# Kernel optimization log

Hardware: AMD Instinct MI355X
Metric: run time of the kernel (lower is better)

## Reference

```python
import jax, jax.numpy as jnp
import numpy as np

INPUT_DIM = 2048
N_TREES = 15
TREE_DEPTH = 3
N_LEAVES = 2 ** TREE_DEPTH          # 8
N_INTERNAL = 2 ** TREE_DEPTH - 1    # 7
PARAM_PER_TREE = N_INTERNAL * (INPUT_DIM + 1) + N_LEAVES * 2  # 14375
BATCH = 32768


def setup_inputs() -> dict:
    key = jax.random.key(0)
    k1, k2, k3 = jax.random.split(key, 3)
    x = jax.random.normal(k1, (BATCH, INPUT_DIM), dtype=jnp.float32)
    tree_params = jax.random.normal(k2, (1, N_TREES * PARAM_PER_TREE), dtype=jnp.float32)
    tree_weights = jax.random.uniform(k3, (1, N_TREES), dtype=jnp.float32)
    return {"x": x, "tree_params": tree_params, "tree_weights": tree_weights}


def reference(x, tree_params, tree_weights):
    D, T, I, L = INPUT_DIM, N_TREES, N_INTERNAL, N_LEAVES
    B = x.shape[0]
    p = tree_params[0].reshape(T, PARAM_PER_TREE)
    split_w = p[:, : I * D].reshape(T, I, D)                       # [T, I, D]
    split_b = p[:, I * D : I * (D + 1)]                            # [T, I]
    leaf_logits = p[:, I * (D + 1) :].reshape(T, L, 2)             # [T, L, 2]

    # One fused GEMM over all trees/nodes: [B, T, I]
    decisions = jax.nn.sigmoid(jnp.einsum('bd,tid->bti', x, split_w) + split_b)

    # Faithful replication of the original gating loop (leaf 0 ungated,
    # internal nodes with child index >= L are no-ops).
    leaf_probs = jnp.ones((B, T, L), dtype=x.dtype)
    for i in range(I):
        left, right = 2 * i + 1, 2 * i + 2
        d = decisions[:, :, i]
        if left < L:
            leaf_probs = leaf_probs.at[:, :, left].multiply(d)
        if right < L:
            leaf_probs = leaf_probs.at[:, :, right].multiply(1.0 - d)

    leaf_probs = leaf_probs / (leaf_probs.sum(axis=-1, keepdims=True) + 1e-8)
    leaf_dist = jax.nn.softmax(leaf_logits, axis=-1)               # [T, L, 2]
    tree_out = jnp.einsum('btl,tlc->btc', leaf_probs, leaf_dist)   # [B, T, 2]
    final_probs = jnp.einsum('btc,t->bc', tree_out, tree_weights[0])
    return final_probs
```

## Files before the change

kernel.cpp:

```cpp
#include <hip/hip_runtime.h>
#include <stdint.h>

#define D_IN    2048
#define NT      15
#define PPT     14359
#define NVALID  60

typedef __bf16   bf16x8 __attribute__((ext_vector_type(8)));
typedef float    f32x4  __attribute__((ext_vector_type(4)));
typedef uint32_t u32x4  __attribute__((ext_vector_type(4)));

#define WAITV8 asm volatile("s_waitcnt vmcnt(8)" ::: "memory")
#define WAITV0 asm volatile("s_waitcnt vmcnt(0)" ::: "memory")
#define WAITL0 asm volatile("s_waitcnt lgkmcnt(0)" ::: "memory")

__global__ __launch_bounds__(256) void prep_split(const float* __restrict__ tp,
                                                  const float* __restrict__ tw,
                                                  unsigned short* __restrict__ bsp,
                                                  float* __restrict__ bias,
                                                  float* __restrict__ coef) {
  int id = blockIdx.x * 256 + threadIdx.x;
  int n = id >> 11;
  int k = id & 2047;
  float v = 0.0f;
  if (n < NVALID) {
    int t = n >> 2, i = n & 3;
    v = tp[t * PPT + i * D_IN + k];
  }
  uint32_t u  = __float_as_uint(v);
  uint32_t hm = u & 0xFFFF0000u;
  float    lo = v - __uint_as_float(hm);
  uint32_t lu = __float_as_uint(lo);
  int ks = k >> 5, f = n >> 4;
  int lane = (n & 15) | (((k >> 3) & 3) << 4);
  int j = k & 7;
  size_t base = ((size_t)(ks * 4 + f) * 2) * 512 + (size_t)lane * 8 + j;
  bsp[base]       = (unsigned short)(u  >> 16);
  bsp[base + 512] = (unsigned short)(lu >> 16);

  if (blockIdx.x == 0) {
    int tid = threadIdx.x;
    if (tid < 64) {
      float b = 0.0f;
      if (tid < NVALID) { int t = tid >> 2, i = tid & 3; b = tp[t * PPT + 14336 + i]; }
      bias[tid] = b;
    } else if (tid < 64 + NT) {
      int t = tid - 64;
      const float* ll = tp + t * PPT + 14343;
      float d0[8], d1[8];
#pragma unroll
      for (int le = 0; le < 8; ++le) {
        float aa = ll[2 * le], bb = ll[2 * le + 1];
        float m = fmaxf(aa, bb);
        float e0 = __expf(aa - m), e1 = __expf(bb - m);
        float inv = 1.0f / (e0 + e1);
        d0[le] = e0 * inv; d1[le] = e1 * inv;
      }
      float w = tw[t];
      float* c = coef + t * 10;
      c[0] = w * (d0[0] + d0[2] + d0[4] + d0[6]);
      c[1] = w * (d1[0] + d1[2] + d1[4] + d1[6]);
      c[2] = w * (d0[1] - d0[2]);
      c[3] = w * (d1[1] - d1[2]);
      c[4] = w * (d0[3] - d0[4]);
      c[5] = w * (d1[3] - d1[4]);
      c[6] = w * (d0[5] - d0[6]);
      c[7] = w * (d1[5] - d1[6]);
      c[8] = w * d0[7];
      c[9] = w * d1[7];
    }
  }
}

__device__ __forceinline__ f32x4 gload4(const float* p) {
  f32x4 r;
  asm volatile("global_load_dwordx4 %0, %1, off" : "=v"(r) : "v"(p) : "memory");
  return r;
}
__device__ __forceinline__ u32x4 dsread16(uint32_t addr) {
  u32x4 r;
  asm volatile("ds_read_b128 %0, %1" : "=v"(r) : "v"(addr) : "memory");
  return r;
}
__device__ __forceinline__ void stage16(const void* g, void* l) {
  __builtin_amdgcn_global_load_lds(
      (const __attribute__((address_space(1))) void*)g,
      (__attribute__((address_space(3))) void*)l, 16, 0, 0);
}

#define CVT_PAIR(P, Q, HW, LW) do {                                   \
    uint32_t _up = __float_as_uint(P), _uq = __float_as_uint(Q);      \
    uint32_t _mp = _up & 0xFFFF0000u, _mq = _uq & 0xFFFF0000u;        \
    (HW) = (_up >> 16) | _mq;                                         \
    float _lp = (P) - __uint_as_float(_mp);                           \
    float _lq = (Q) - __uint_as_float(_mq);                           \
    (LW) = (__float_as_uint(_lp) >> 16) |                             \
           (__float_as_uint(_lq) & 0xFFFF0000u);                      \
  } while (0)

__device__ __forceinline__ void cvt_hilo(const f32x4 A, const f32x4 B,
                                         bf16x8& hi, bf16x8& lo) {
  u32x4 hw, lw;
  CVT_PAIR(A[0], A[1], hw[0], lw[0]);
  CVT_PAIR(A[2], A[3], hw[1], lw[1]);
  CVT_PAIR(B[0], B[1], hw[2], lw[2]);
  CVT_PAIR(B[2], B[3], hw[3], lw[3]);
  hi = __builtin_bit_cast(bf16x8, hw);
  lo = __builtin_bit_cast(bf16x8, lw);
}

#define ITERATION(tt, BUF, RC, WAIT8, ISSUE)                                   \
  {                                                                            \
    if (WAIT8) { WAITV8; } else { WAITV0; }                                    \
    __builtin_amdgcn_sched_barrier(0);                                         \
    __builtin_amdgcn_s_barrier();                                              \
    const uint32_t bb = sbase + (BUF) * 16384 + l16;                           \
    u32x4 bf[16];                                                              \
    _Pragma("unroll")                                                          \
    for (int h = 0; h < 2; ++h)                                                \
      _Pragma("unroll")                                                        \
      for (int f = 0; f < 4; ++f)                                              \
        _Pragma("unroll")                                                      \
        for (int p2 = 0; p2 < 2; ++p2)                                         \
          bf[h * 8 + f * 2 + p2] = dsread16(bb + h * 8192 + f * 2048 + p2 * 1024); \
    bf16x8 ah0, al0, ah1, al1;                                                 \
    cvt_hilo(RC[0], RC[1], ah0, al0);                                          \
    cvt_hilo(RC[2], RC[3], ah1, al1);                                          \
    WAITL0;                                                                    \
    __builtin_amdgcn_sched_barrier(0);                                         \
    if (ISSUE) {                                                               \
      const int t2 = (tt) + 2;                                                 \
      const char* gsrc = bspb + (size_t)t2 * 16384 + w4096l16;                 \
      char* ldst = sBgen + (((BUF) + 2) % 3) * 16384 + w4096;                  \
      _Pragma("unroll")                                                        \
      for (int q = 0; q < 4; ++q) stage16(gsrc + q * 1024, ldst + q * 1024);   \
      const float* ap = xbase + t2 * 64;                                       \
      RC[0] = gload4(ap);      RC[1] = gload4(ap + 4);                         \
      RC[2] = gload4(ap + 32); RC[3] = gload4(ap + 36);                        \
    }                                                                          \
    _Pragma("unroll")                                                          \
    for (int f = 0; f < 4; ++f) {                                              \
      bf16x8 bh = __builtin_bit_cast(bf16x8, bf[f * 2]);                       \
      bf16x8 bl = __builtin_bit_cast(bf16x8, bf[f * 2 + 1]);                   \
      acc[f] = __builtin_amdgcn_mfma_f32_16x16x32_bf16(ah0, bh, acc[f], 0,0,0);\
      acc[f] = __builtin_amdgcn_mfma_f32_16x16x32_bf16(al0, bh, acc[f], 0,0,0);\
      acc[f] = __builtin_amdgcn_mfma_f32_16x16x32_bf16(ah0, bl, acc[f], 0,0,0);\
    }                                                                          \
    _Pragma("unroll")                                                          \
    for (int f = 0; f < 4; ++f) {                                              \
      bf16x8 bh = __builtin_bit_cast(bf16x8, bf[8 + f * 2]);                   \
      bf16x8 bl = __builtin_bit_cast(bf16x8, bf[8 + f * 2 + 1]);               \
      acc[f] = __builtin_amdgcn_mfma_f32_16x16x32_bf16(ah1, bh, acc[f], 0,0,0);\
      acc[f] = __builtin_amdgcn_mfma_f32_16x16x32_bf16(al1, bh, acc[f], 0,0,0);\
      acc[f] = __builtin_amdgcn_mfma_f32_16x16x32_bf16(ah1, bl, acc[f], 0,0,0);\
    }                                                                          \
  }

__global__ __launch_bounds__(256) void tree_fused(
    const float* __restrict__ x,
    const unsigned short* __restrict__ bsp,
    const float* __restrict__ bias,
    const float* __restrict__ coef,
    float* __restrict__ out)
{
  __shared__ __align__(1024) unsigned char sB[3 * 16384];
  __shared__ float strips[4][16][65];

  const int tid = threadIdx.x;
  const int w   = tid >> 6;
  const int l   = tid & 63;
  const int rl  = l & 15;
  const int g   = l >> 4;
  const int l16 = l * 16;
  const int w4096 = w * 4096;
  const int w4096l16 = w4096 + l16;

  const int rowTile = blockIdx.x * 64 + w * 16;
  const float* xbase = x + (size_t)(rowTile + rl) * D_IN + g * 8;
  const char* bspb = (const char*)bsp;
  char* sBgen = (char*)&sB[0];
  const uint32_t sbase = (uint32_t)(uintptr_t)sBgen;

  f32x4 acc[4] = {};
  f32x4 rA[4], rB[4];

  {
    const char* g0 = bspb + w4096l16;
    char* d0 = sBgen + w4096;
#pragma unroll
    for (int q = 0; q < 4; ++q) stage16(g0 + q * 1024, d0 + q * 1024);
    const float* ap = xbase;
    rA[0] = gload4(ap);      rA[1] = gload4(ap + 4);
    rA[2] = gload4(ap + 32); rA[3] = gload4(ap + 36);
    const char* g1 = bspb + 16384 + w4096l16;
    char* d1 = sBgen + 16384 + w4096;
#pragma unroll
    for (int q = 0; q < 4; ++q) stage16(g1 + q * 1024, d1 + q * 1024);
    const float* ap1 = xbase + 64;
    rB[0] = gload4(ap1);      rB[1] = gload4(ap1 + 4);
    rB[2] = gload4(ap1 + 32); rB[3] = gload4(ap1 + 36);
  }

  for (int tb = 0; tb < 30; tb += 6) {
    ITERATION(tb + 0, 0, rA, true, true);
    ITERATION(tb + 1, 1, rB, true, true);
    ITERATION(tb + 2, 2, rA, true, true);
    ITERATION(tb + 3, 0, rB, true, true);
    ITERATION(tb + 4, 1, rA, true, true);
    ITERATION(tb + 5, 2, rB, true, true);
  }
  ITERATION(30, 0, rA, true, false);
  ITERATION(31, 1, rB, false, false);

#pragma unroll
  for (int f = 0; f < 4; ++f)
#pragma unroll
    for (int r = 0; r < 4; ++r)
      strips[w][4 * g + r][16 * f + rl] = acc[f][r];
  WAITL0;

  float o0 = 0.0f, o1 = 0.0f;
#pragma unroll
  for (int jt = 0; jt < 4; ++jt) {
    int t = g + 4 * jt;
    if (t < NT) {
      const float* cf = coef + t * 10;
      float dd[4];
#pragma unroll
      for (int i = 0; i < 4; ++i) {
        float z = strips[w][rl][4 * t + i] + bias[4 * t + i];
        dd[i] = 1.0f / (1.0f + __expf(-z));
      }
      float s = 1.0f / (4.0f + dd[3] + 1e-8f);
      o0 += s * (cf[0] + dd[0] * cf[2] + dd[1] * cf[4] + dd[2] * cf[6] + dd[3] * cf[8]);
      o1 += s * (cf[1] + dd[0] * cf[3] + dd[1] * cf[5] + dd[2] * cf[7] + dd[3] * cf[9]);
    }
  }
  o0 += __shfl_xor(o0, 16); o0 += __shfl_xor(o0, 32);
  o1 += __shfl_xor(o1, 16); o1 += __shfl_xor(o1, 32);
  if (l < 16) {
    ((float2*)out)[rowTile + rl] = make_float2(o0, o1);
  }
}

extern "C" void kernel_launch(void* const* d_in, const int* in_sizes, int n_in,
                              void* d_out, int out_size, void* d_ws, size_t ws_size,
                              hipStream_t stream) {
  (void)in_sizes; (void)n_in; (void)out_size; (void)ws_size;
  const float* x  = (const float*)d_in[0];
  const float* tp = (const float*)d_in[1];
  const float* tw = (const float*)d_in[2];
  float* out = (float*)d_out;

  unsigned short* bsp = (unsigned short*)d_ws;
  float* bias = (float*)((char*)d_ws + 524288);
  float* coef = (float*)((char*)d_ws + 524288 + 256);

  prep_split<<<512, 256, 0, stream>>>(tp, tw, bsp, bias, coef);
  tree_fused<<<512, 256, 0, stream>>>(x, bsp, bias, coef, out);
}
```

Baseline: 56.41 us.

## Fuse split-weight prep into main kernel, converting weights per tile in-loop

Removes the separate prep kernel that converted split weights into a bf16 hi/lo swizzled workspace layout, along with the bias and coefficient precompute. Each block now loads raw fp32 weights from the parameter tensor, splits them into bf16 hi/lo in registers, and writes them to the LDS triple buffer inside the pipelined loop. Bias and leaf coefficients are computed per block into shared memory. This saves a kernel launch and the workspace round trip. In exchange every block redoes the weight conversion, issues more register loads and conversion ALU work per iteration, and the async global-to-LDS copies become register-staged LDS writes.

```diff
diff --git a/kernel.cpp b/kernel.cpp
--- a/kernel.cpp
+++ b/kernel.cpp
@@ -13,64 +13,7 @@
 #define WAITV8 asm volatile("s_waitcnt vmcnt(8)" ::: "memory")
 #define WAITV0 asm volatile("s_waitcnt vmcnt(0)" ::: "memory")
 #define WAITL0 asm volatile("s_waitcnt lgkmcnt(0)" ::: "memory")
-
-__global__ __launch_bounds__(256) void prep_split(const float* __restrict__ tp,
-                                                  const float* __restrict__ tw,
-                                                  unsigned short* __restrict__ bsp,
-                                                  float* __restrict__ bias,
-                                                  float* __restrict__ coef) {
-  int id = blockIdx.x * 256 + threadIdx.x;
-  int n = id >> 11;
-  int k = id & 2047;
-  float v = 0.0f;
-  if (n < NVALID) {
-    int t = n >> 2, i = n & 3;
-    v = tp[t * PPT + i * D_IN + k];
-  }
-  uint32_t u  = __float_as_uint(v);
-  uint32_t hm = u & 0xFFFF0000u;
-  float    lo = v - __uint_as_float(hm);
-  uint32_t lu = __float_as_uint(lo);
-  int ks = k >> 5, f = n >> 4;
-  int lane = (n & 15) | (((k >> 3) & 3) << 4);
-  int j = k & 7;
-  size_t base = ((size_t)(ks * 4 + f) * 2) * 512 + (size_t)lane * 8 + j;
-  bsp[base]       = (unsigned short)(u  >> 16);
-  bsp[base + 512] = (unsigned short)(lu >> 16);
-
-  if (blockIdx.x == 0) {
-    int tid = threadIdx.x;
-    if (tid < 64) {
-      float b = 0.0f;
-      if (tid < NVALID) { int t = tid >> 2, i = tid & 3; b = tp[t * PPT + 14336 + i]; }
-      bias[tid] = b;
-    } else if (tid < 64 + NT) {
-      int t = tid - 64;
-      const float* ll = tp + t * PPT + 14343;
-      float d0[8], d1[8];
-#pragma unroll
-      for (int le = 0; le < 8; ++le) {
-        float aa = ll[2 * le], bb = ll[2 * le + 1];
-        float m = fmaxf(aa, bb);
-        float e0 = __expf(aa - m), e1 = __expf(bb - m);
-        float inv = 1.0f / (e0 + e1);
-        d0[le] = e0 * inv; d1[le] = e1 * inv;
-      }
-      float w = tw[t];
-      float* c = coef + t * 10;
-      c[0] = w * (d0[0] + d0[2] + d0[4] + d0[6]);
-      c[1] = w * (d1[0] + d1[2] + d1[4] + d1[6]);
-      c[2] = w * (d0[1] - d0[2]);
-      c[3] = w * (d1[1] - d1[2]);
-      c[4] = w * (d0[3] - d0[4]);
-      c[5] = w * (d1[3] - d1[4]);
-      c[6] = w * (d0[5] - d0[6]);
-      c[7] = w * (d1[5] - d1[6]);
-      c[8] = w * d0[7];
-      c[9] = w * d1[7];
-    }
-  }
-}
+#define SCHEDB __builtin_amdgcn_sched_barrier(0)
 
 __device__ __forceinline__ f32x4 gload4(const float* p) {
   f32x4 r;
@@ -82,10 +25,8 @@
   asm volatile("ds_read_b128 %0, %1" : "=v"(r) : "v"(addr) : "memory");
   return r;
 }
-__device__ __forceinline__ void stage16(const void* g, void* l) {
-  __builtin_amdgcn_global_load_lds(
-      (const __attribute__((address_space(1))) void*)g,
-      (__attribute__((address_space(3))) void*)l, 16, 0, 0);
+__device__ __forceinline__ void dswrite16(uint32_t addr, u32x4 v) {
+  asm volatile("ds_write_b128 %0, %1" :: "v"(addr), "v"(v) : "memory");
 }
 
 #define CVT_PAIR(P, Q, HW, LW) do {                                   \
@@ -98,73 +39,77 @@
            (__float_as_uint(_lq) & 0xFFFF0000u);                      \
   } while (0)
 
-__device__ __forceinline__ void cvt_hilo(const f32x4 A, const f32x4 B,
-                                         bf16x8& hi, bf16x8& lo) {
-  u32x4 hw, lw;
-  CVT_PAIR(A[0], A[1], hw[0], lw[0]);
-  CVT_PAIR(A[2], A[3], hw[1], lw[1]);
-  CVT_PAIR(B[0], B[1], hw[2], lw[2]);
-  CVT_PAIR(B[2], B[3], hw[3], lw[3]);
-  hi = __builtin_bit_cast(bf16x8, hw);
-  lo = __builtin_bit_cast(bf16x8, lw);
-}
-
-#define ITERATION(tt, BUF, RC, WAIT8, ISSUE)                                   \
+__device__ __forceinline__ void cvt8(const f32x4 A, const f32x4 B,
+                                     u32x4& hi, u32x4& lo) {
+  CVT_PAIR(A[0], A[1], hi[0], lo[0]);
+  CVT_PAIR(A[2], A[3], hi[1], lo[1]);
+  CVT_PAIR(B[0], B[1], hi[2], lo[2]);
+  CVT_PAIR(B[2], B[3], hi[3], lo[3]);
+}
+
+#define ITERATION(tt, BUF, WBUF, RC, WA, WB, ISSUE, ENDSTAGE, ENDV0)           \
   {                                                                            \
-    if (WAIT8) { WAITV8; } else { WAITV0; }                                    \
-    __builtin_amdgcn_sched_barrier(0);                                         \
     __builtin_amdgcn_s_barrier();                                              \
     const uint32_t bb = sbase + (BUF) * 16384 + l16;                           \
-    u32x4 bf[16];                                                              \
+    u32x4 bfr[16];                                                             \
     _Pragma("unroll")                                                          \
-    for (int h = 0; h < 2; ++h)                                                \
-      _Pragma("unroll")                                                        \
-      for (int f = 0; f < 4; ++f)                                              \
-        _Pragma("unroll")                                                      \
-        for (int p2 = 0; p2 < 2; ++p2)                                         \
-          bf[h * 8 + f * 2 + p2] = dsread16(bb + h * 8192 + f * 2048 + p2 * 1024); \
-    bf16x8 ah0, al0, ah1, al1;                                                 \
-    cvt_hilo(RC[0], RC[1], ah0, al0);                                          \
-    cvt_hilo(RC[2], RC[3], ah1, al1);                                          \
-    WAITL0;                                                                    \
-    __builtin_amdgcn_sched_barrier(0);                                         \
+    for (int q = 0; q < 16; ++q) bfr[q] = dsread16(bb + q * 1024);             \
+    u32x4 ah0, al0, ah1, al1;                                                  \
+    cvt8(RC[0], RC[1], ah0, al0);                                              \
+    cvt8(RC[2], RC[3], ah1, al1);                                              \
+    WAITL0; SCHEDB;                                                            \
     if (ISSUE) {                                                               \
       const int t2 = (tt) + 2;                                                 \
-      const char* gsrc = bspb + (size_t)t2 * 16384 + w4096l16;                 \
-      char* ldst = sBgen + (((BUF) + 2) % 3) * 16384 + w4096;                  \
-      _Pragma("unroll")                                                        \
-      for (int q = 0; q < 4; ++q) stage16(gsrc + q * 1024, ldst + q * 1024);   \
+      WA[0] = gload4(wp0 + t2 * 64);  WA[1] = gload4(wp0 + t2 * 64 + 4);       \
+      WA[2] = gload4(wp1 + t2 * 64);  WA[3] = gload4(wp1 + t2 * 64 + 4);       \
       const float* ap = xbase + t2 * 64;                                       \
       RC[0] = gload4(ap);      RC[1] = gload4(ap + 4);                         \
       RC[2] = gload4(ap + 32); RC[3] = gload4(ap + 36);                        \
     }                                                                          \
     _Pragma("unroll")                                                          \
     for (int f = 0; f < 4; ++f) {                                              \
-      bf16x8 bh = __builtin_bit_cast(bf16x8, bf[f * 2]);                       \
-      bf16x8 bl = __builtin_bit_cast(bf16x8, bf[f * 2 + 1]);                   \
-      acc[f] = __builtin_amdgcn_mfma_f32_16x16x32_bf16(ah0, bh, acc[f], 0,0,0);\
-      acc[f] = __builtin_amdgcn_mfma_f32_16x16x32_bf16(al0, bh, acc[f], 0,0,0);\
-      acc[f] = __builtin_amdgcn_mfma_f32_16x16x32_bf16(ah0, bl, acc[f], 0,0,0);\
+      bf16x8 bh = __builtin_bit_cast(bf16x8, bfr[f * 2]);                      \
+      bf16x8 bl = __builtin_bit_cast(bf16x8, bfr[f * 2 + 1]);                  \
+      bf16x8 Ah = __builtin_bit_cast(bf16x8, ah0);                             \
+      bf16x8 Al = __builtin_bit_cast(bf16x8, al0);                             \
+      acc[f] = __builtin_amdgcn_mfma_f32_16x16x32_bf16(Ah, bh, acc[f], 0,0,0); \
+      acc[f] = __builtin_amdgcn_mfma_f32_16x16x32_bf16(Al, bh, acc[f], 0,0,0); \
+      acc[f] = __builtin_amdgcn_mfma_f32_16x16x32_bf16(Ah, bl, acc[f], 0,0,0); \
     }                                                                          \
     _Pragma("unroll")                                                          \
     for (int f = 0; f < 4; ++f) {                                              \
-      bf16x8 bh = __builtin_bit_cast(bf16x8, bf[8 + f * 2]);                   \
-      bf16x8 bl = __builtin_bit_cast(bf16x8, bf[8 + f * 2 + 1]);               \
-      acc[f] = __builtin_amdgcn_mfma_f32_16x16x32_bf16(ah1, bh, acc[f], 0,0,0);\
-      acc[f] = __builtin_amdgcn_mfma_f32_16x16x32_bf16(al1, bh, acc[f], 0,0,0);\
-      acc[f] = __builtin_amdgcn_mfma_f32_16x16x32_bf16(ah1, bl, acc[f], 0,0,0);\
+      bf16x8 bh = __builtin_bit_cast(bf16x8, bfr[8 + f * 2]);                  \
+      bf16x8 bl = __builtin_bit_cast(bf16x8, bfr[8 + f * 2 + 1]);              \
+      bf16x8 Ah = __builtin_bit_cast(bf16x8, ah1);                             \
+      bf16x8 Al = __builtin_bit_cast(bf16x8, al1);                             \
+      acc[f] = __builtin_amdgcn_mfma_f32_16x16x32_bf16(Ah, bh, acc[f], 0,0,0); \
+      acc[f] = __builtin_amdgcn_mfma_f32_16x16x32_bf16(Al, bh, acc[f], 0,0,0); \
+      acc[f] = __builtin_amdgcn_mfma_f32_16x16x32_bf16(Ah, bl, acc[f], 0,0,0); \
+    }                                                                          \
+    if (ENDSTAGE) {                                                            \
+      if (ENDV0) { WAITV0; } else { WAITV8; }                                  \
+      SCHEDB;                                                                  \
+      f32x4 w2 = WB[2] * vmask, w3 = WB[3] * vmask;                            \
+      u32x4 h0, l0, h1, l1;                                                    \
+      cvt8(WB[0], WB[1], h0, l0);                                              \
+      cvt8(w2, w3, h1, l1);                                                    \
+      const uint32_t wb_ = sbase + (WBUF) * 16384 + w4096 + l16;               \
+      dswrite16(wb_,        h0);  dswrite16(wb_ + 1024, l0);                   \
+      dswrite16(wb_ + 2048, h1);  dswrite16(wb_ + 3072, l1);                   \
+      WAITL0; SCHEDB;                                                          \
     }                                                                          \
   }
 
 __global__ __launch_bounds__(256) void tree_fused(
     const float* __restrict__ x,
-    const unsigned short* __restrict__ bsp,
-    const float* __restrict__ bias,
-    const float* __restrict__ coef,
+    const float* __restrict__ tp,
+    const float* __restrict__ tw,
     float* __restrict__ out)
 {
   __shared__ __align__(1024) unsigned char sB[3 * 16384];
   __shared__ float strips[4][16][65];
+  __shared__ float sBias[64];
+  __shared__ float sCoef[160];
 
   const int tid = threadIdx.x;
   const int w   = tid >> 6;
@@ -173,44 +118,86 @@
   const int g   = l >> 4;
   const int l16 = l * 16;
   const int w4096 = w * 4096;
-  const int w4096l16 = w4096 + l16;
+
+  if (tid < 64) {
+    float b = 0.0f;
+    if (tid < NVALID) { int t = tid >> 2, i = tid & 3; b = tp[t * PPT + 14336 + i]; }
+    sBias[tid] = b;
+  } else if (tid < 64 + NT) {
+    int t = tid - 64;
+    const float* ll = tp + t * PPT + 14343;
+    float d0[8], d1[8];
+#pragma unroll
+    for (int le = 0; le < 8; ++le) {
+      float aa = ll[2 * le], bb = ll[2 * le + 1];
+      float m = fmaxf(aa, bb);
+      float e0 = __expf(aa - m), e1 = __expf(bb - m);
+      float inv = 1.0f / (e0 + e1);
+      d0[le] = e0 * inv; d1[le] = e1 * inv;
+    }
+    float ww = tw[t];
+    float* c = sCoef + t * 10;
+    c[0] = ww * (d0[0] + d0[2] + d0[4] + d0[6]);
+    c[1] = ww * (d1[0] + d1[2] + d1[4] + d1[6]);
+    c[2] = ww * (d0[1] - d0[2]);
+    c[3] = ww * (d1[1] - d1[2]);
+    c[4] = ww * (d0[3] - d0[4]);
+    c[5] = ww * (d1[3] - d1[4]);
+    c[6] = ww * (d0[5] - d0[6]);
+    c[7] = ww * (d1[5] - d1[6]);
+    c[8] = ww * d0[7];
+    c[9] = ww * d1[7];
+  }
+  __syncthreads();
+
+  const int h  = w >> 1;
+  const int f0 = 2 * (w & 1);
+  const int n0 = 16 * f0 + rl;
+  const int n1 = n0 + 16;
+  const float vmask = (n1 < NVALID) ? 1.0f : 0.0f;
+  const int coloff = h * 32 + g * 8;
+  const float* wp0 = tp + (size_t)(n0 >> 2) * PPT + (n0 & 3) * D_IN + coloff;
+  const float* wp1r = tp + (size_t)(n1 >> 2) * PPT + (n1 & 3) * D_IN + coloff;
+  const float* wp1 = (n1 < NVALID) ? wp1r : tp;
 
   const int rowTile = blockIdx.x * 64 + w * 16;
   const float* xbase = x + (size_t)(rowTile + rl) * D_IN + g * 8;
-  const char* bspb = (const char*)bsp;
-  char* sBgen = (char*)&sB[0];
-  const uint32_t sbase = (uint32_t)(uintptr_t)sBgen;
+  const uint32_t sbase = (uint32_t)(uintptr_t)&sB[0];
 
   f32x4 acc[4] = {};
   f32x4 rA[4], rB[4];
+  f32x4 wWa[4], wWb[4];
 
   {
-    const char* g0 = bspb + w4096l16;
-    char* d0 = sBgen + w4096;
-#pragma unroll
-    for (int q = 0; q < 4; ++q) stage16(g0 + q * 1024, d0 + q * 1024);
-    const float* ap = xbase;
-    rA[0] = gload4(ap);      rA[1] = gload4(ap + 4);
-    rA[2] = gload4(ap + 32); rA[3] = gload4(ap + 36);
-    const char* g1 = bspb + 16384 + w4096l16;
-    char* d1 = sBgen + 16384 + w4096;
-#pragma unroll
-    for (int q = 0; q < 4; ++q) stage16(g1 + q * 1024, d1 + q * 1024);
-    const float* ap1 = xbase + 64;
-    rB[0] = gload4(ap1);      rB[1] = gload4(ap1 + 4);
-    rB[2] = gload4(ap1 + 32); rB[3] = gload4(ap1 + 36);
+    wWa[0] = gload4(wp0);      wWa[1] = gload4(wp0 + 4);
+    wWa[2] = gload4(wp1);      wWa[3] = gload4(wp1 + 4);
+    rA[0] = gload4(xbase);      rA[1] = gload4(xbase + 4);
+    rA[2] = gload4(xbase + 32); rA[3] = gload4(xbase + 36);
+    wWb[0] = gload4(wp0 + 64);  wWb[1] = gload4(wp0 + 68);
+    wWb[2] = gload4(wp1 + 64);  wWb[3] = gload4(wp1 + 68);
+    rB[0] = gload4(xbase + 64); rB[1] = gload4(xbase + 68);
+    rB[2] = gload4(xbase + 96); rB[3] = gload4(xbase + 100);
+    WAITV8; SCHEDB;
+    f32x4 w2 = wWa[2] * vmask, w3 = wWa[3] * vmask;
+    u32x4 h0, l0, h1, l1;
+    cvt8(wWa[0], wWa[1], h0, l0);
+    cvt8(w2, w3, h1, l1);
+    const uint32_t wb_ = sbase + w4096 + l16;
+    dswrite16(wb_,        h0);  dswrite16(wb_ + 1024, l0);
+    dswrite16(wb_ + 2048, h1);  dswrite16(wb_ + 3072, l1);
+    WAITL0; SCHEDB;
   }
 
   for (int tb = 0; tb < 30; tb += 6) {
-    ITERATION(tb + 0, 0, rA, true, true);
-    ITERATION(tb + 1, 1, rB, true, true);
-    ITERATION(tb + 2, 2, rA, true, true);
-    ITERATION(tb + 3, 0, rB, true, true);
-    ITERATION(tb + 4, 1, rA, true, true);
-    ITERATION(tb + 5, 2, rB, true, true);
-  }
-  ITERATION(30, 0, rA, true, false);
-  ITERATION(31, 1, rB, false, false);
+    ITERATION(tb + 0, 0, 1, rA, wWa, wWb, 1, 1, 0);
+    ITERATION(tb + 1, 1, 2, rB, wWb, wWa, 1, 1, 0);
+    ITERATION(tb + 2, 2, 0, rA, wWa, wWb, 1, 1, 0);
+    ITERATION(tb + 3, 0, 1, rB, wWb, wWa, 1, 1, 0);
+    ITERATION(tb + 4, 1, 2, rA, wWa, wWb, 1, 1, 0);
+    ITERATION(tb + 5, 2, 0, rB, wWb, wWa, 1, 1, 0);
+  }
+  ITERATION(30, 0, 1, rA, wWa, wWb, 0, 1, 1);
+  ITERATION(31, 1, 2, rB, wWb, wWa, 0, 0, 0);
 
 #pragma unroll
   for (int f = 0; f < 4; ++f)
@@ -224,11 +211,11 @@
   for (int jt = 0; jt < 4; ++jt) {
     int t = g + 4 * jt;
     if (t < NT) {
-      const float* cf = coef + t * 10;
+      const float* cf = sCoef + t * 10;
       float dd[4];
 #pragma unroll
       for (int i = 0; i < 4; ++i) {
-        float z = strips[w][rl][4 * t + i] + bias[4 * t + i];
+        float z = strips[w][rl][4 * t + i] + sBias[4 * t + i];
         dd[i] = 1.0f / (1.0f + __expf(-z));
       }
       float s = 1.0f / (4.0f + dd[3] + 1e-8f);
@@ -246,16 +233,11 @@
 extern "C" void kernel_launch(void* const* d_in, const int* in_sizes, int n_in,
                               void* d_out, int out_size, void* d_ws, size_t ws_size,
                               hipStream_t stream) {
-  (void)in_sizes; (void)n_in; (void)out_size; (void)ws_size;
+  (void)in_sizes; (void)n_in; (void)out_size; (void)d_ws; (void)ws_size;
   const float* x  = (const float*)d_in[0];
   const float* tp = (const float*)d_in[1];
   const float* tw = (const float*)d_in[2];
   float* out = (float*)d_out;
 
-  unsigned short* bsp = (unsigned short*)d_ws;
-  float* bias = (float*)((char*)d_ws + 524288);
-  float* coef = (float*)((char*)d_ws + 524288 + 256);
-
-  prep_split<<<512, 256, 0, stream>>>(tp, tw, bsp, bias, coef);
-  tree_fused<<<512, 256, 0, stream>>>(x, bsp, bias, coef, out);
-}
+  tree_fused<<<512, 256, 0, stream>>>(x, tp, tw, out);
+}
```

New measurement: 66.94 us. 18.7% more time.
